# Performance work log

Hardware: AMD Instinct MI355X
Metric: run time of the kernel (lower is better)

Reference implementation:

```python
import jax, jax.numpy as jnp
import numpy as np

N_NODES = 50000
N_EDGES = 800000
F_IN, C1, C2 = 128, 100, 4
NEG_SLOPE = 0.2  # PyG GATConv default LeakyReLU slope


def setup_inputs() -> dict:
    key = jax.random.key(0)
    ks = jax.random.split(key, 10)
    def glorot(k, shape):
        fan = sum(shape)
        return jax.random.normal(k, shape, jnp.float32) * jnp.sqrt(2.0 / fan)
    return {
        "x": jax.random.normal(ks[0], (N_NODES, F_IN), jnp.float32),
        "edge_index": jax.random.randint(ks[1], (2, N_EDGES), 0, N_NODES, jnp.int64),
        "W1": glorot(ks[2], (F_IN, C1)),
        "att_src1": glorot(ks[3], (1, C1)),
        "att_dst1": glorot(ks[4], (1, C1)),
        "b1": jnp.zeros((C1,), jnp.float32),
        "W2": glorot(ks[5], (C1, C2)),
        "att_src2": glorot(ks[6], (1, C2)),
        "att_dst2": glorot(ks[7], (1, C2)),
        "b2": jnp.zeros((C2,), jnp.float32),
    }


def _gat_conv(x, edge_index, W, att_src, att_dst, bias):
    """PyG GATConv (heads=1, concat=True, add_self_loops=True), eval mode."""
    n = x.shape[0]
    # add self loops
    loop = jnp.arange(n, dtype=edge_index.dtype)
    src = jnp.concatenate([edge_index[0], loop])
    dst = jnp.concatenate([edge_index[1], loop])
    h = x @ W                                   # [N, C]
    a_src = (h * att_src[0]).sum(-1)            # [N]
    a_dst = (h * att_dst[0]).sum(-1)            # [N]
    e = jax.nn.leaky_relu(a_src[src] + a_dst[dst], NEG_SLOPE)  # [E+N]
    # segment softmax over destination neighborhoods
    m = jax.ops.segment_max(e, dst, num_segments=n)            # [N]
    w = jnp.exp(e - m[dst])
    denom = jax.ops.segment_sum(w, dst, num_segments=n)        # [N]
    alpha = w / denom[dst]                                     # [E+N]
    msg = h[src] * alpha[:, None]                              # [E+N, C]
    out = jax.ops.segment_sum(msg, dst, num_segments=n)        # [N, C]
    return out + bias


def reference(x, edge_index, W1, att_src1, att_dst1, b1, W2, att_src2, att_dst2, b2):
    h = _gat_conv(x, edge_index, W1, att_src1, att_dst1, b1)
    h = jax.nn.relu(h)  # dropout is identity in eval mode
    h = _gat_conv(h, edge_index, W2, att_src2, att_dst2, b2)
    return jax.nn.log_softmax(h, axis=1)
```

## Files before the change

### kernel.cpp

```cpp
#include <hip/hip_runtime.h>
#include <math.h>

#define N_NODES 50000
#define N_EDGES 800000
#define F_IN 128
#define C1 100
#define C1D 50
#define C2 4
#define NEG 0.2f
#define DEGCAP 64
#define NBUCK 196
#define BCAP 4608
#define BSTR 16
#define PA_NB 196
#define PA_CHUNK 1021
#define GEMM_NB 782
#define W1P 136

typedef __attribute__((ext_vector_type(8))) _Float16 f16x8;
typedef __attribute__((ext_vector_type(2))) _Float16 f16x2;
typedef __attribute__((ext_vector_type(4))) float f32x4;

__device__ __forceinline__ float leaky(float v) { return v > 0.f ? v : NEG * v; }

__device__ __forceinline__ unsigned pkh(float a, float b) {
    auto p = __builtin_amdgcn_cvt_pkrtz(a, b);
    return __builtin_bit_cast(unsigned, p);
}
__device__ __forceinline__ float h_lo(unsigned g) {
    f16x2 p = __builtin_bit_cast(f16x2, g);
    return (float)p[0];
}
__device__ __forceinline__ float h_hi(unsigned g) {
    f16x2 p = __builtin_bit_cast(f16x2, g);
    return (float)p[1];
}
__device__ __forceinline__ float rlanef(float v, int l) {
    return __int_as_float(__builtin_amdgcn_readlane(__float_as_int(v), l));
}

__global__ __launch_bounds__(256)
void k_gemm_scatter(const float* __restrict__ x, const float* __restrict__ W1,
                    const float* __restrict__ as1, const float* __restrict__ ad1,
                    unsigned* __restrict__ h1b, float* __restrict__ a_src1,
                    float* __restrict__ a_dst1, const int* __restrict__ ei,
                    int* __restrict__ bcnt, unsigned* __restrict__ breg) {
    __shared__ union SM {
        struct { int lcnt[NBUCK]; int lbase[NBUCK]; } pa;
        unsigned short w1[112 * W1P];
    } sm;
    int tid = threadIdx.x;
    if (blockIdx.x < PA_NB) {
        int* lcnt = sm.pa.lcnt;
        int* lbase = sm.pa.lbase;
        if (tid < NBUCK) lcnt[tid] = 0;
        __syncthreads();
        int g0 = blockIdx.x * PA_CHUNK;
        int4 s4[4], d4[4];
        int off[4][4];
        bool val[4];
#pragma unroll
        for (int it = 0; it < 4; ++it) {
            int local = it * 256 + tid;
            int g = g0 + local;
            val[it] = (local < PA_CHUNK) && (g < N_EDGES / 4);
            if (val[it]) {
                s4[it] = *(const int4*)(ei + (long)g * 4);
                d4[it] = *(const int4*)(ei + N_EDGES + (long)g * 4);
                off[it][0] = atomicAdd(&lcnt[d4[it].x >> 8], 1);
                off[it][1] = atomicAdd(&lcnt[d4[it].y >> 8], 1);
                off[it][2] = atomicAdd(&lcnt[d4[it].z >> 8], 1);
                off[it][3] = atomicAdd(&lcnt[d4[it].w >> 8], 1);
            }
        }
        __syncthreads();
        if (tid < NBUCK) {
            int c = lcnt[tid];
            lbase[tid] = c ? atomicAdd(&bcnt[tid * BSTR], c) : 0;
        }
        __syncthreads();
#pragma unroll
        for (int it = 0; it < 4; ++it) {
            if (!val[it]) continue;
            { int b = d4[it].x >> 8; int p = lbase[b] + off[it][0];
              if (p < BCAP) breg[b * BCAP + p] = ((unsigned)s4[it].x << 8) | ((unsigned)d4[it].x & 255u); }
            { int b = d4[it].y >> 8; int p = lbase[b] + off[it][1];
              if (p < BCAP) breg[b * BCAP + p] = ((unsigned)s4[it].y << 8) | ((unsigned)d4[it].y & 255u); }
            { int b = d4[it].z >> 8; int p = lbase[b] + off[it][2];
              if (p < BCAP) breg[b * BCAP + p] = ((unsigned)s4[it].z << 8) | ((unsigned)d4[it].z & 255u); }
            { int b = d4[it].w >> 8; int p = lbase[b] + off[it][3];
              if (p < BCAP) breg[b * BCAP + p] = ((unsigned)s4[it].w << 8) | ((unsigned)d4[it].w & 255u); }
        }
        return;
    }
    unsigned short* w1s = sm.w1;
    for (int i = tid; i < 12800; i += 256) {
        int k = i / 100, n = i - k * 100;
        _Float16 hv = (_Float16)W1[i];
        w1s[n * W1P + k] = __builtin_bit_cast(unsigned short, hv);
    }
    for (int i = tid; i < 12 * 128; i += 256) {
        int n = 100 + (i >> 7), k = i & 127;
        w1s[n * W1P + k] = 0;
    }
    __syncthreads();

    int half = blockIdx.x - PA_NB;
    int node0 = half * 64;
    int wave = tid >> 6, lane = tid & 63;
    int mrow = lane & 15;
    int quad = lane >> 4;
    int na = node0 + wave * 16 + mrow;
    bool vrow = na < N_NODES;
    const float* px = x + (long)na * F_IN + quad * 8;

    f16x8 afr[4];
#pragma unroll
    for (int kc = 0; kc < 4; ++kc) {
        float4 v0 = make_float4(0.f, 0.f, 0.f, 0.f), v1 = v0;
        if (vrow) {
            v0 = *(const float4*)(px + kc * 32);
            v1 = *(const float4*)(px + kc * 32 + 4);
        }
        union { unsigned u[4]; f16x8 h; } t;
        t.u[0] = pkh(v0.x, v0.y);
        t.u[1] = pkh(v0.z, v0.w);
        t.u[2] = pkh(v1.x, v1.y);
        t.u[3] = pkh(v1.z, v1.w);
        afr[kc] = t.h;
    }

    f32x4 acc[7];
#pragma unroll
    for (int nt = 0; nt < 7; ++nt) {
        const _Float16* pb = (const _Float16*)w1s + (nt * 16 + mrow) * W1P + quad * 8;
        f32x4 a = {0.f, 0.f, 0.f, 0.f};
#pragma unroll
        for (int kc = 0; kc < 4; ++kc) {
            f16x8 bfr = *(const f16x8*)(pb + kc * 32);
            a = __builtin_amdgcn_mfma_f32_16x16x32_f16(afr[kc], bfr, a, 0, 0, 0);
        }
        acc[nt] = a;
    }

    float ps[4] = {0.f, 0.f, 0.f, 0.f}, pd[4] = {0.f, 0.f, 0.f, 0.f};
#pragma unroll
    for (int nt = 0; nt < 7; ++nt) {
        int col = nt * 16 + mrow;
        float av = 0.f, dv = 0.f;
        if (col < C1) { av = as1[col]; dv = ad1[col]; }
#pragma unroll
        for (int r = 0; r < 4; ++r) {
            ps[r] += acc[nt][r] * av;
            pd[r] += acc[nt][r] * dv;
        }
    }
#pragma unroll
    for (int r = 0; r < 4; ++r) {
#pragma unroll
        for (int off = 1; off < 16; off <<= 1) {
            ps[r] += __shfl_xor(ps[r], off);
            pd[r] += __shfl_xor(pd[r], off);
        }
    }
    if (mrow == 0) {
#pragma unroll
        for (int r = 0; r < 4; ++r) {
            int n = node0 + wave * 16 + quad * 4 + r;
            if (n < N_NODES) { a_src1[n] = ps[r]; a_dst1[n] = pd[r]; }
        }
    }

#pragma unroll
    for (int nt = 0; nt < 7; ++nt) {
#pragma unroll
        for (int r = 0; r < 4; ++r) {
            float v = acc[nt][r];
            float o = __shfl_xor(v, 1);
            int col = nt * 16 + mrow;
            int n = node0 + wave * 16 + quad * 4 + r;
            if ((mrow & 1) == 0 && col < C1 && n < N_NODES) {
                h1b[(long)n * C1D + (col >> 1)] = pkh(v, o);
            }
        }
    }
}

__global__ __launch_bounds__(512) void k_bucket(const unsigned* __restrict__ breg,
                                                const int* __restrict__ bcnt,
                                                int* __restrict__ cnt,
                                                unsigned short* __restrict__ slots) {
    __shared__ int dcnt[256];
    int b = blockIdx.x, tid = threadIdx.x;
    if (tid < 256) dcnt[tid] = 0;
    __syncthreads();
    int n = min(bcnt[b * BSTR], BCAP);
    const unsigned* reg = breg + b * BCAP;
    for (int e = tid; e < n; e += 512) {
        unsigned p = reg[e];
        int d8 = p & 255;
        int slot = atomicAdd(&dcnt[d8], 1);
        if (slot < DEGCAP) slots[(((b << 8) + d8) << 6) + slot] = (unsigned short)(p >> 8);
    }
    __syncthreads();
    if (tid < 256) {
        int d = (b << 8) + tid;
        if (d < N_NODES) cnt[d] = dcnt[tid];
    }
}

__global__ __launch_bounds__(256) void k_agg1(const unsigned* __restrict__ h1b, const float* __restrict__ a_src,
                                              const float* __restrict__ a_dst, const int* __restrict__ cnt,
                                              const unsigned short* __restrict__ slots, const float* __restrict__ b1,
                                              const float* __restrict__ W2, const float* __restrict__ as2,
                                              const float* __restrict__ ad2, float4* __restrict__ recs) {
    __shared__ float sW2[C1 * C2];
    __shared__ float sB1[C1];
    int tid = threadIdx.x;
    for (int f = tid; f < C1 * C2; f += 256) sW2[f] = W2[f];
    if (tid < C1) sB1[tid] = b1[tid];
    __syncthreads();
    int wave = tid >> 6, lane = tid & 63;
    int d = blockIdx.x * 4 + wave;
    if (d >= N_NODES) return;
    int cn = min(cnt[d], DEGCAP);
    float ad = a_dst[d];
    int c = lane;
    bool act = c < C1D;
    int cc = act ? c : 0;

    float wself = __expf(leaky(a_src[d] + ad));
    unsigned gs = h1b[(long)d * C1D + cc];
    float accL = wself * h_lo(gs), accH = wself * h_hi(gs);
    float lsum = (lane == 0) ? wself : 0.f;

    int sreg = 0; float wreg = 0.f;
    if (lane < cn) {
        sreg = (int)slots[d * DEGCAP + lane];
        wreg = __expf(leaky(a_src[sreg] + ad));
        lsum += wreg;
    }

    unsigned ga[8], gb[8];
#define LD(buf, e) { int sv_ = __builtin_amdgcn_readlane(sreg, (e)); \
                     buf = h1b[(long)sv_ * C1D + cc]; }
#define CONSUME(buf, e) if ((e) < cn) { float w_ = rlanef(wreg, (e)); \
                     accL = fmaf(h_lo(buf), w_, accL); accH = fmaf(h_hi(buf), w_, accH); }

#pragma unroll
    for (int i = 0; i < 8; ++i) LD(ga[i], i);
#pragma unroll
    for (int bp = 0; bp < 4; ++bp) {
        const int b0 = 2 * bp, b1i = 2 * bp + 1;
        if (b0 * 8 >= cn) break;
        if (b1i * 8 < cn) {
#pragma unroll
            for (int i = 0; i < 8; ++i) LD(gb[i], b1i * 8 + i);
        }
#pragma unroll
        for (int i = 0; i < 8; ++i) CONSUME(ga[i], b0 * 8 + i);
        if (b1i * 8 >= cn) break;
        if ((b1i + 1) * 8 < cn) {
#pragma unroll
            for (int i = 0; i < 8; ++i) LD(ga[i], (b1i + 1) * 8 + i);
        }
#pragma unroll
        for (int i = 0; i < 8; ++i) CONSUME(gb[i], b1i * 8 + i);
    }
#undef LD
#undef CONSUME

    for (int off = 32; off; off >>= 1) lsum += __shfl_xor(lsum, off);
    float invl = 1.f / lsum;
    float p0 = 0.f, p1 = 0.f, p2 = 0.f, p3 = 0.f;
    if (act) {
        float v0 = fmaxf(accL * invl + sB1[2 * c], 0.f);
        float v1 = fmaxf(accH * invl + sB1[2 * c + 1], 0.f);
        const float* w0 = &sW2[(2 * c) * 4];
        p0 = v0 * w0[0] + v1 * w0[4];
        p1 = v0 * w0[1] + v1 * w0[5];
        p2 = v0 * w0[2] + v1 * w0[6];
        p3 = v0 * w0[3] + v1 * w0[7];
    }
    for (int off = 32; off; off >>= 1) {
        p0 += __shfl_xor(p0, off);
        p1 += __shfl_xor(p1, off);
        p2 += __shfl_xor(p2, off);
        p3 += __shfl_xor(p3, off);
    }
    if (lane == 0) {
        recs[2 * d] = make_float4(p0, p1, p2, p3);
        float s2 = p0 * as2[0] + p1 * as2[1] + p2 * as2[2] + p3 * as2[3];
        float t2 = p0 * ad2[0] + p1 * ad2[1] + p2 * ad2[2] + p3 * ad2[3];
        recs[2 * d + 1] = make_float4(s2, t2, 0.f, 0.f);
    }
}

__global__ __launch_bounds__(256) void k_agg2(const float4* __restrict__ recs, const int* __restrict__ cnt,
                                              const unsigned short* __restrict__ slots, const float* __restrict__ b2,
                                              float4* __restrict__ out) {
    int wave = threadIdx.x >> 6, lane = threadIdx.x & 63;
    int grp = lane >> 4, li = lane & 15;
    for (int d = blockIdx.x * 16 + wave * 4 + grp; d < N_NODES; d += gridDim.x * 16) {
        int cn = min(cnt[d], DEGCAP);
        float ad = recs[2 * d + 1].y;
        float l = 0.f, a0 = 0.f, a1 = 0.f, a2 = 0.f, a3 = 0.f;
        if (li == 0) {
            float4 r1 = recs[2 * d + 1];
            float w = __expf(leaky(r1.x + ad));
            float4 hv = recs[2 * d];
            l = w; a0 = w * hv.x; a1 = w * hv.y; a2 = w * hv.z; a3 = w * hv.w;
        }
        for (int j = li; j < cn; j += 16) {
            int s = (int)slots[d * DEGCAP + j];
            float4 r1 = recs[2 * s + 1];
            float w = __expf(leaky(r1.x + ad));
            l += w;
            float4 hv = recs[2 * s];
            a0 += w * hv.x; a1 += w * hv.y; a2 += w * hv.z; a3 += w * hv.w;
        }
#pragma unroll
        for (int off = 8; off; off >>= 1) {
            l += __shfl_xor(l, off);
            a0 += __shfl_xor(a0, off);
            a1 += __shfl_xor(a1, off);
            a2 += __shfl_xor(a2, off);
            a3 += __shfl_xor(a3, off);
        }
        if (li == 0) {
            float invl = 1.f / l;
            float v0 = a0 * invl + b2[0];
            float v1 = a1 * invl + b2[1];
            float v2 = a2 * invl + b2[2];
            float v3 = a3 * invl + b2[3];
            float mm = fmaxf(fmaxf(v0, v1), fmaxf(v2, v3));
            float ls = logf(__expf(v0 - mm) + __expf(v1 - mm) + __expf(v2 - mm) + __expf(v3 - mm)) + mm;
            out[d] = make_float4(v0 - ls, v1 - ls, v2 - ls, v3 - ls);
        }
    }
}

extern "C" void kernel_launch(void* const* d_in, const int* in_sizes, int n_in,
                              void* d_out, int out_size, void* d_ws, size_t ws_size,
                              hipStream_t stream) {
    const float* x   = (const float*)d_in[0];
    const int*   ei  = (const int*)d_in[1];
    const float* W1  = (const float*)d_in[2];
    const float* as1 = (const float*)d_in[3];
    const float* ad1 = (const float*)d_in[4];
    const float* b1  = (const float*)d_in[5];
    const float* W2  = (const float*)d_in[6];
    const float* as2 = (const float*)d_in[7];
    const float* ad2 = (const float*)d_in[8];
    const float* b2  = (const float*)d_in[9];
    float4* out = (float4*)d_out;

    char* w = (char*)d_ws;
    unsigned* h1b    = (unsigned*)(w + 0);
    float*    a_src1 = (float*)(w + 10000000);
    float*    a_dst1 = (float*)(w + 10200000);
    float4*   recs   = (float4*)(w + 10400000);
    int*      cnt    = (int*)(w + 12000000);
    int*      bcnt   = (int*)(w + 12200000);
    unsigned short* slots = (unsigned short*)(w + 12216000);
    unsigned* breg   = (unsigned*)(w + 18616000);

    hipMemsetAsync(bcnt, 0, NBUCK * BSTR * 4, stream);
    k_gemm_scatter<<<PA_NB + GEMM_NB, 256, 0, stream>>>(x, W1, as1, ad1, h1b, a_src1, a_dst1,
                                                        ei, bcnt, breg);
    k_bucket<<<NBUCK, 512, 0, stream>>>(breg, bcnt, cnt, slots);
    k_agg1<<<(N_NODES + 3) / 4, 256, 0, stream>>>(h1b, a_src1, a_dst1, cnt, slots, b1, W2, as2, ad2,
                                                  recs);
    k_agg2<<<1563, 256, 0, stream>>>(recs, cnt, slots, b2, out);
}
```

Measured before the change: 155.3 us.

## Precompute layer-1 edge weights in bucket kernel; halve GEMM block count

```diff
diff --git a/kernel.cpp b/kernel.cpp
--- a/kernel.cpp
+++ b/kernel.cpp
@@ -14,7 +14,7 @@
 #define BSTR 16
 #define PA_NB 196
 #define PA_CHUNK 1021
-#define GEMM_NB 782
+#define GEMM_NB 391
 #define W1P 136
 
 typedef __attribute__((ext_vector_type(8))) _Float16 f16x8;
@@ -106,81 +106,84 @@
     __syncthreads();
 
     int half = blockIdx.x - PA_NB;
-    int node0 = half * 64;
     int wave = tid >> 6, lane = tid & 63;
     int mrow = lane & 15;
     int quad = lane >> 4;
-    int na = node0 + wave * 16 + mrow;
-    bool vrow = na < N_NODES;
-    const float* px = x + (long)na * F_IN + quad * 8;
-
-    f16x8 afr[4];
-#pragma unroll
-    for (int kc = 0; kc < 4; ++kc) {
-        float4 v0 = make_float4(0.f, 0.f, 0.f, 0.f), v1 = v0;
-        if (vrow) {
-            v0 = *(const float4*)(px + kc * 32);
-            v1 = *(const float4*)(px + kc * 32 + 4);
-        }
-        union { unsigned u[4]; f16x8 h; } t;
-        t.u[0] = pkh(v0.x, v0.y);
-        t.u[1] = pkh(v0.z, v0.w);
-        t.u[2] = pkh(v1.x, v1.y);
-        t.u[3] = pkh(v1.z, v1.w);
-        afr[kc] = t.h;
-    }
-
-    f32x4 acc[7];
-#pragma unroll
-    for (int nt = 0; nt < 7; ++nt) {
-        const _Float16* pb = (const _Float16*)w1s + (nt * 16 + mrow) * W1P + quad * 8;
-        f32x4 a = {0.f, 0.f, 0.f, 0.f};
+
+    for (int p2 = 0; p2 < 2; ++p2) {
+        int node0 = half * 128 + p2 * 64;
+        int na = node0 + wave * 16 + mrow;
+        bool vrow = na < N_NODES;
+        const float* px = x + (long)na * F_IN + quad * 8;
+
+        f16x8 afr[4];
 #pragma unroll
         for (int kc = 0; kc < 4; ++kc) {
-            f16x8 bfr = *(const f16x8*)(pb + kc * 32);
-            a = __builtin_amdgcn_mfma_f32_16x16x32_f16(afr[kc], bfr, a, 0, 0, 0);
-        }
-        acc[nt] = a;
-    }
-
-    float ps[4] = {0.f, 0.f, 0.f, 0.f}, pd[4] = {0.f, 0.f, 0.f, 0.f};
-#pragma unroll
-    for (int nt = 0; nt < 7; ++nt) {
-        int col = nt * 16 + mrow;
-        float av = 0.f, dv = 0.f;
-        if (col < C1) { av = as1[col]; dv = ad1[col]; }
+            float4 v0 = make_float4(0.f, 0.f, 0.f, 0.f), v1 = v0;
+            if (vrow) {
+                v0 = *(const float4*)(px + kc * 32);
+                v1 = *(const float4*)(px + kc * 32 + 4);
+            }
+            union { unsigned u[4]; f16x8 h; } t;
+            t.u[0] = pkh(v0.x, v0.y);
+            t.u[1] = pkh(v0.z, v0.w);
+            t.u[2] = pkh(v1.x, v1.y);
+            t.u[3] = pkh(v1.z, v1.w);
+            afr[kc] = t.h;
+        }
+
+        f32x4 acc[7];
+#pragma unroll
+        for (int nt = 0; nt < 7; ++nt) {
+            const _Float16* pb = (const _Float16*)w1s + (nt * 16 + mrow) * W1P + quad * 8;
+            f32x4 a = {0.f, 0.f, 0.f, 0.f};
+#pragma unroll
+            for (int kc = 0; kc < 4; ++kc) {
+                f16x8 bfr = *(const f16x8*)(pb + kc * 32);
+                a = __builtin_amdgcn_mfma_f32_16x16x32_f16(afr[kc], bfr, a, 0, 0, 0);
+            }
+            acc[nt] = a;
+        }
+
+        float ps[4] = {0.f, 0.f, 0.f, 0.f}, pd[4] = {0.f, 0.f, 0.f, 0.f};
+#pragma unroll
+        for (int nt = 0; nt < 7; ++nt) {
+            int col = nt * 16 + mrow;
+            float av = 0.f, dv = 0.f;
+            if (col < C1) { av = as1[col]; dv = ad1[col]; }
+#pragma unroll
+            for (int r = 0; r < 4; ++r) {
+                ps[r] += acc[nt][r] * av;
+                pd[r] += acc[nt][r] * dv;
+            }
+        }
 #pragma unroll
         for (int r = 0; r < 4; ++r) {
-            ps[r] += acc[nt][r] * av;
-            pd[r] += acc[nt][r] * dv;
-        }
-    }
-#pragma unroll
-    for (int r = 0; r < 4; ++r) {
-#pragma unroll
-        for (int off = 1; off < 16; off <<= 1) {
-            ps[r] += __shfl_xor(ps[r], off);
-            pd[r] += __shfl_xor(pd[r], off);
-        }
-    }
-    if (mrow == 0) {
-#pragma unroll
-        for (int r = 0; r < 4; ++r) {
-            int n = node0 + wave * 16 + quad * 4 + r;
-            if (n < N_NODES) { a_src1[n] = ps[r]; a_dst1[n] = pd[r]; }
-        }
-    }
-
-#pragma unroll
-    for (int nt = 0; nt < 7; ++nt) {
-#pragma unroll
-        for (int r = 0; r < 4; ++r) {
-            float v = acc[nt][r];
-            float o = __shfl_xor(v, 1);
-            int col = nt * 16 + mrow;
-            int n = node0 + wave * 16 + quad * 4 + r;
-            if ((mrow & 1) == 0 && col < C1 && n < N_NODES) {
-                h1b[(long)n * C1D + (col >> 1)] = pkh(v, o);
+#pragma unroll
+            for (int off = 1; off < 16; off <<= 1) {
+                ps[r] += __shfl_xor(ps[r], off);
+                pd[r] += __shfl_xor(pd[r], off);
+            }
+        }
+        if (mrow == 0) {
+#pragma unroll
+            for (int r = 0; r < 4; ++r) {
+                int n = node0 + wave * 16 + quad * 4 + r;
+                if (n < N_NODES) { a_src1[n] = ps[r]; a_dst1[n] = pd[r]; }
+            }
+        }
+
+#pragma unroll
+        for (int nt = 0; nt < 7; ++nt) {
+#pragma unroll
+            for (int r = 0; r < 4; ++r) {
+                float v = acc[nt][r];
+                float o = __shfl_xor(v, 1);
+                int col = nt * 16 + mrow;
+                int n = node0 + wave * 16 + quad * 4 + r;
+                if ((mrow & 1) == 0 && col < C1 && n < N_NODES) {
+                    h1b[(long)n * C1D + (col >> 1)] = pkh(v, o);
+                }
             }
         }
     }
@@ -188,19 +191,32 @@
 
 __global__ __launch_bounds__(512) void k_bucket(const unsigned* __restrict__ breg,
                                                 const int* __restrict__ bcnt,
+                                                const float* __restrict__ a_src1,
+                                                const float* __restrict__ a_dst1,
                                                 int* __restrict__ cnt,
-                                                unsigned short* __restrict__ slots) {
+                                                unsigned short* __restrict__ slots,
+                                                float* __restrict__ wslots) {
     __shared__ int dcnt[256];
+    __shared__ float sdst[256];
     int b = blockIdx.x, tid = threadIdx.x;
-    if (tid < 256) dcnt[tid] = 0;
+    if (tid < 256) {
+        dcnt[tid] = 0;
+        int d = (b << 8) + tid;
+        sdst[tid] = (d < N_NODES) ? a_dst1[d] : 0.f;
+    }
     __syncthreads();
     int n = min(bcnt[b * BSTR], BCAP);
     const unsigned* reg = breg + b * BCAP;
     for (int e = tid; e < n; e += 512) {
         unsigned p = reg[e];
         int d8 = p & 255;
+        int src = (int)(p >> 8);
         int slot = atomicAdd(&dcnt[d8], 1);
-        if (slot < DEGCAP) slots[(((b << 8) + d8) << 6) + slot] = (unsigned short)(p >> 8);
+        if (slot < DEGCAP) {
+            long idx = (((long)(b << 8) + d8) << 6) + slot;
+            slots[idx] = (unsigned short)src;
+            wslots[idx] = __expf(leaky(a_src1[src] + sdst[d8]));
+        }
     }
     __syncthreads();
     if (tid < 256) {
@@ -211,7 +227,8 @@
 
 __global__ __launch_bounds__(256) void k_agg1(const unsigned* __restrict__ h1b, const float* __restrict__ a_src,
                                               const float* __restrict__ a_dst, const int* __restrict__ cnt,
-                                              const unsigned short* __restrict__ slots, const float* __restrict__ b1,
+                                              const unsigned short* __restrict__ slots,
+                                              const float* __restrict__ wslots, const float* __restrict__ b1,
                                               const float* __restrict__ W2, const float* __restrict__ as2,
                                               const float* __restrict__ ad2, float4* __restrict__ recs) {
     __shared__ float sW2[C1 * C2];
@@ -224,27 +241,23 @@
     int d = blockIdx.x * 4 + wave;
     if (d >= N_NODES) return;
     int cn = min(cnt[d], DEGCAP);
-    float ad = a_dst[d];
     int c = lane;
     bool act = c < C1D;
     int cc = act ? c : 0;
 
-    float wself = __expf(leaky(a_src[d] + ad));
+    int sreg = (int)slots[(long)d * DEGCAP + lane];
+    float wrow = wslots[(long)d * DEGCAP + lane];
+    float wself = __expf(leaky(a_src[d] + a_dst[d]));
     unsigned gs = h1b[(long)d * C1D + cc];
+
     float accL = wself * h_lo(gs), accH = wself * h_hi(gs);
     float lsum = (lane == 0) ? wself : 0.f;
-
-    int sreg = 0; float wreg = 0.f;
-    if (lane < cn) {
-        sreg = (int)slots[d * DEGCAP + lane];
-        wreg = __expf(leaky(a_src[sreg] + ad));
-        lsum += wreg;
-    }
+    if (lane < cn) lsum += wrow;
 
     unsigned ga[8], gb[8];
 #define LD(buf, e) { int sv_ = __builtin_amdgcn_readlane(sreg, (e)); \
                      buf = h1b[(long)sv_ * C1D + cc]; }
-#define CONSUME(buf, e) if ((e) < cn) { float w_ = rlanef(wreg, (e)); \
+#define CONSUME(buf, e) if ((e) < cn) { float w_ = rlanef(wrow, (e)); \
                      accL = fmaf(h_lo(buf), w_, accL); accH = fmaf(h_hi(buf), w_, accH); }
 
 #pragma unroll
@@ -312,7 +325,7 @@
             l = w; a0 = w * hv.x; a1 = w * hv.y; a2 = w * hv.z; a3 = w * hv.w;
         }
         for (int j = li; j < cn; j += 16) {
-            int s = (int)slots[d * DEGCAP + j];
+            int s = (int)slots[(long)d * DEGCAP + j];
             float4 r1 = recs[2 * s + 1];
             float w = __expf(leaky(r1.x + ad));
             l += w;
@@ -364,12 +377,13 @@
     int*      bcnt   = (int*)(w + 12200000);
     unsigned short* slots = (unsigned short*)(w + 12216000);
     unsigned* breg   = (unsigned*)(w + 18616000);
+    float*    wslots = (float*)(w + 22228672);
 
     hipMemsetAsync(bcnt, 0, NBUCK * BSTR * 4, stream);
     k_gemm_scatter<<<PA_NB + GEMM_NB, 256, 0, stream>>>(x, W1, as1, ad1, h1b, a_src1, a_dst1,
                                                         ei, bcnt, breg);
-    k_bucket<<<NBUCK, 512, 0, stream>>>(breg, bcnt, cnt, slots);
-    k_agg1<<<(N_NODES + 3) / 4, 256, 0, stream>>>(h1b, a_src1, a_dst1, cnt, slots, b1, W2, as2, ad2,
-                                                  recs);
+    k_bucket<<<NBUCK, 512, 0, stream>>>(breg, bcnt, a_src1, a_dst1, cnt, slots, wslots);
+    k_agg1<<<(N_NODES + 3) / 4, 256, 0, stream>>>(h1b, a_src1, a_dst1, cnt, slots, wslots, b1, W2,
+                                                  as2, ad2, recs);
     k_agg2<<<1563, 256, 0, stream>>>(recs, cnt, slots, b2, out);
 }
```

New measurement: 164.5 us. 1.06x slower.

## Replace global atomic bucket offsets with per-block bucket regions and counts

Applied to the files above, without the earlier changes.

```diff
diff --git a/kernel.cpp b/kernel.cpp
--- a/kernel.cpp
+++ b/kernel.cpp
@@ -10,10 +10,9 @@
 #define NEG 0.2f
 #define DEGCAP 64
 #define NBUCK 196
-#define BCAP 4608
-#define BSTR 16
 #define PA_NB 196
 #define PA_CHUNK 1021
+#define PBC 64
 #define GEMM_NB 782
 #define W1P 136
 
@@ -44,18 +43,18 @@
                     const float* __restrict__ as1, const float* __restrict__ ad1,
                     unsigned* __restrict__ h1b, float* __restrict__ a_src1,
                     float* __restrict__ a_dst1, const int* __restrict__ ei,
-                    int* __restrict__ bcnt, unsigned* __restrict__ breg) {
+                    int* __restrict__ cnt2d, unsigned* __restrict__ breg2) {
     __shared__ union SM {
-        struct { int lcnt[NBUCK]; int lbase[NBUCK]; } pa;
+        int lcnt[NBUCK];
         unsigned short w1[112 * W1P];
     } sm;
     int tid = threadIdx.x;
     if (blockIdx.x < PA_NB) {
-        int* lcnt = sm.pa.lcnt;
-        int* lbase = sm.pa.lbase;
+        int* lcnt = sm.lcnt;
+        int blk = blockIdx.x;
         if (tid < NBUCK) lcnt[tid] = 0;
         __syncthreads();
-        int g0 = blockIdx.x * PA_CHUNK;
+        int g0 = blk * PA_CHUNK;
         int4 s4[4], d4[4];
         int off[4][4];
         bool val[4];
@@ -74,22 +73,18 @@
             }
         }
         __syncthreads();
-        if (tid < NBUCK) {
-            int c = lcnt[tid];
-            lbase[tid] = c ? atomicAdd(&bcnt[tid * BSTR], c) : 0;
-        }
-        __syncthreads();
+        if (tid < NBUCK) cnt2d[tid * PA_NB + blk] = lcnt[tid];
 #pragma unroll
         for (int it = 0; it < 4; ++it) {
             if (!val[it]) continue;
-            { int b = d4[it].x >> 8; int p = lbase[b] + off[it][0];
-              if (p < BCAP) breg[b * BCAP + p] = ((unsigned)s4[it].x << 8) | ((unsigned)d4[it].x & 255u); }
-            { int b = d4[it].y >> 8; int p = lbase[b] + off[it][1];
-              if (p < BCAP) breg[b * BCAP + p] = ((unsigned)s4[it].y << 8) | ((unsigned)d4[it].y & 255u); }
-            { int b = d4[it].z >> 8; int p = lbase[b] + off[it][2];
-              if (p < BCAP) breg[b * BCAP + p] = ((unsigned)s4[it].z << 8) | ((unsigned)d4[it].z & 255u); }
-            { int b = d4[it].w >> 8; int p = lbase[b] + off[it][3];
-              if (p < BCAP) breg[b * BCAP + p] = ((unsigned)s4[it].w << 8) | ((unsigned)d4[it].w & 255u); }
+            { int b = d4[it].x >> 8; int p = off[it][0];
+              if (p < PBC) breg2[((long)b * PA_NB + blk) * PBC + p] = ((unsigned)s4[it].x << 8) | ((unsigned)d4[it].x & 255u); }
+            { int b = d4[it].y >> 8; int p = off[it][1];
+              if (p < PBC) breg2[((long)b * PA_NB + blk) * PBC + p] = ((unsigned)s4[it].y << 8) | ((unsigned)d4[it].y & 255u); }
+            { int b = d4[it].z >> 8; int p = off[it][2];
+              if (p < PBC) breg2[((long)b * PA_NB + blk) * PBC + p] = ((unsigned)s4[it].z << 8) | ((unsigned)d4[it].z & 255u); }
+            { int b = d4[it].w >> 8; int p = off[it][3];
+              if (p < PBC) breg2[((long)b * PA_NB + blk) * PBC + p] = ((unsigned)s4[it].w << 8) | ((unsigned)d4[it].w & 255u); }
         }
         return;
     }
@@ -186,21 +181,26 @@
     }
 }
 
-__global__ __launch_bounds__(512) void k_bucket(const unsigned* __restrict__ breg,
-                                                const int* __restrict__ bcnt,
+__global__ __launch_bounds__(512) void k_bucket(const unsigned* __restrict__ breg2,
+                                                const int* __restrict__ cnt2d,
                                                 int* __restrict__ cnt,
                                                 unsigned short* __restrict__ slots) {
     __shared__ int dcnt[256];
+    __shared__ int scnt[PA_NB];
     int b = blockIdx.x, tid = threadIdx.x;
     if (tid < 256) dcnt[tid] = 0;
+    if (tid < PA_NB) scnt[tid] = min(cnt2d[b * PA_NB + tid], PBC);
     __syncthreads();
-    int n = min(bcnt[b * BSTR], BCAP);
-    const unsigned* reg = breg + b * BCAP;
-    for (int e = tid; e < n; e += 512) {
-        unsigned p = reg[e];
-        int d8 = p & 255;
-        int slot = atomicAdd(&dcnt[d8], 1);
-        if (slot < DEGCAP) slots[(((b << 8) + d8) << 6) + slot] = (unsigned short)(p >> 8);
+    const unsigned* base = breg2 + (long)b * PA_NB * PBC;
+    for (int f = tid; f < PA_NB * PBC; f += 512) {
+        int blk = f >> 6;
+        int j = f & (PBC - 1);
+        if (j < scnt[blk]) {
+            unsigned p = base[f];
+            int d8 = p & 255;
+            int slot = atomicAdd(&dcnt[d8], 1);
+            if (slot < DEGCAP) slots[(((b << 8) + d8) << 6) + slot] = (unsigned short)(p >> 8);
+        }
     }
     __syncthreads();
     if (tid < 256) {
@@ -236,7 +236,7 @@
 
     int sreg = 0; float wreg = 0.f;
     if (lane < cn) {
-        sreg = (int)slots[d * DEGCAP + lane];
+        sreg = (int)slots[(long)d * DEGCAP + lane];
         wreg = __expf(leaky(a_src[sreg] + ad));
         lsum += wreg;
     }
@@ -312,7 +312,7 @@
             l = w; a0 = w * hv.x; a1 = w * hv.y; a2 = w * hv.z; a3 = w * hv.w;
         }
         for (int j = li; j < cn; j += 16) {
-            int s = (int)slots[d * DEGCAP + j];
+            int s = (int)slots[(long)d * DEGCAP + j];
             float4 r1 = recs[2 * s + 1];
             float w = __expf(leaky(r1.x + ad));
             l += w;
@@ -361,15 +361,14 @@
     float*    a_dst1 = (float*)(w + 10200000);
     float4*   recs   = (float4*)(w + 10400000);
     int*      cnt    = (int*)(w + 12000000);
-    int*      bcnt   = (int*)(w + 12200000);
     unsigned short* slots = (unsigned short*)(w + 12216000);
-    unsigned* breg   = (unsigned*)(w + 18616000);
-
-    hipMemsetAsync(bcnt, 0, NBUCK * BSTR * 4, stream);
+    int*      cnt2d  = (int*)(w + 18616000);
+    unsigned* breg2  = (unsigned*)(w + 18769664);
+
     k_gemm_scatter<<<PA_NB + GEMM_NB, 256, 0, stream>>>(x, W1, as1, ad1, h1b, a_src1, a_dst1,
-                                                        ei, bcnt, breg);
-    k_bucket<<<NBUCK, 512, 0, stream>>>(breg, bcnt, cnt, slots);
-    k_agg1<<<(N_NODES + 3) / 4, 256, 0, stream>>>(h1b, a_src1, a_dst1, cnt, slots, b1, W2, as2, ad2,
-                                                  recs);
+                                                        ei, cnt2d, breg2);
+    k_bucket<<<NBUCK, 512, 0, stream>>>(breg2, cnt2d, cnt, slots);
+    k_agg1<<<(N_NODES + 3) / 4, 256, 0, stream>>>(h1b, a_src1, a_dst1, cnt, slots, b1, W2,
+                                                  as2, ad2, recs);
     k_agg2<<<1563, 256, 0, stream>>>(recs, cnt, slots, b2, out);
 }
```

Measured after the change: 158.0 us. No clear change (+1.8%).
